# Kernel optimization log

Measured on AMD Instinct MI355X. Metric: run time of the kernel, lower is better.

Reference implementation:

```python
import jax, jax.numpy as jnp
import numpy as np

BLOCK_SIZE = 256
N_EMBD = 768
HEAD_SIZE = 768  # == n_embd so RoPE table (dim=n_embd) matches channel pairing


def _rope_tables(T, dim, theta0=10000.0):
    # compute_freq(dim=n_embd, seq_len=block_size, theta_0=10000):
    # theta_j = theta0^(-2j/dim), angle[t, j] = t * theta_j
    j = jnp.arange(dim // 2, dtype=jnp.float32)
    theta = jnp.float32(theta0) ** (-2.0 * j / jnp.float32(dim))
    ang = jnp.arange(T, dtype=jnp.float32)[:, None] * theta[None, :]  # [T, dim/2]
    return jnp.cos(ang), jnp.sin(ang)


def _apply_rope(t, cos, sin):
    # t: [B, T, D]; pair adjacent channels (2j, 2j+1) as complex, rotate.
    B, T, D = t.shape
    tr = t.reshape(B, T, D // 2, 2)
    re, im = tr[..., 0], tr[..., 1]
    out_re = re * cos[None] - im * sin[None]
    out_im = re * sin[None] + im * cos[None]
    return jnp.stack([out_re, out_im], axis=-1).reshape(B, T, D)


def setup_inputs() -> dict:
    key = jax.random.key(0)
    k1, k2, k3, k4 = jax.random.split(key, 4)
    B, T = 128, BLOCK_SIZE
    x = jax.random.normal(k1, (B, T, N_EMBD), dtype=jnp.float32)
    Wq = jax.random.normal(k2, (N_EMBD, HEAD_SIZE), dtype=jnp.float32) * 0.02
    Wk = jax.random.normal(k3, (N_EMBD, HEAD_SIZE), dtype=jnp.float32) * 0.02
    Wv = jax.random.normal(k4, (N_EMBD, HEAD_SIZE), dtype=jnp.float32) * 0.02
    return {"x": x, "Wq": Wq, "Wk": Wk, "Wv": Wv}


def reference(x, Wq, Wk, Wv):
    B, T, C = x.shape
    q = x @ Wq  # [B, T, D]
    k = x @ Wk
    v = x @ Wv
    cos, sin = _rope_tables(T, HEAD_SIZE)
    q = _apply_rope(q, cos, sin)
    k = _apply_rope(k, cos, sin)
    scale = jnp.float32(HEAD_SIZE) ** -0.5
    wei = jnp.einsum('bqd,bkd->bqk', q, k) * scale  # [B, T, T]
    causal = jnp.tril(jnp.ones((T, T), dtype=bool))
    wei = jnp.where(causal[None], wei, -jnp.inf)
    wei = jax.nn.softmax(wei, axis=-1)
    # dropout(p=0.2) is identity in eval/deterministic baseline
    out = jnp.einsum('bqk,bkd->bqd', wei, v)  # [B, T, D]
    return out
```

## Files before the change

kernel.cpp:

```cpp
#include <hip/hip_runtime.h>
#include <hip/hip_bf16.h>
#include <stdint.h>


typedef __attribute__((ext_vector_type(8))) short short8;
typedef __attribute__((ext_vector_type(4))) short short4v;
typedef __attribute__((ext_vector_type(4))) float f32x4;

__device__ __forceinline__ short f2bf(float f) {
    uint32_t u = __float_as_uint(f);
    u += 0x7fffu + ((u >> 16) & 1u);
    return (short)(u >> 16);
}

__global__ __launch_bounds__(256) void cvt_x(const float* __restrict__ x,
                                             short* __restrict__ xb) {
    long i = ((long)blockIdx.x * 256 + threadIdx.x) * 4;
    f32x4 v = *(const f32x4*)(x + i);
    short4v o;
    o.x = f2bf(v.x); o.y = f2bf(v.y); o.z = f2bf(v.z); o.w = f2bf(v.w);
    *(short4v*)(xb + i) = o;
}

__global__ __launch_bounds__(256) void cvt_wt(const float* __restrict__ W,
                                              short* __restrict__ Wt) {
    __shared__ float tile[32][33];
    int d0 = blockIdx.x * 32, c0 = blockIdx.y * 32;
    int tr = threadIdx.x >> 5, tc = threadIdx.x & 31;
    #pragma unroll
    for (int i = 0; i < 32; i += 8)
        tile[tr + i][tc] = W[(long)(c0 + tr + i) * 768 + d0 + tc];
    __syncthreads();
    #pragma unroll
    for (int i = 0; i < 32; i += 8)
        Wt[(long)(d0 + tr + i) * 768 + c0 + tc] = f2bf(tile[tc][tr + i]);
}

__global__ __launch_bounds__(256) void rope_tab(float2* __restrict__ rt) {
    int i = blockIdx.x * 256 + threadIdx.x;
    int t = i / 384, j = i - t * 384;
    const float CE = -0.034603417655f;
    float th = exp2f((float)j * CE);
    float s, c;
    sincosf((float)t * th, &s, &c);
    rt[i] = make_float2(c, s);
}

__global__ __launch_bounds__(512, 2)
void qkv256(const short* __restrict__ A, const short* __restrict__ B,
            short* __restrict__ Q, short* __restrict__ Kb,
            short* __restrict__ Vt, const float2* __restrict__ rt) {
    int p = blockIdx.x;
    int c = p & 7, j = p >> 3;
    int st = j / 9;
    int bx = j - st * 9;
    int by = c * 16 + st;
    const int m0 = by * 256, n0 = bx * 256;

    __shared__ short lA[2][256 * 64];
    __shared__ short lB[2][256 * 64];

    const int tid = threadIdx.x;
    const int w = tid >> 6, lane = tid & 63;
    const int wm = (w >> 2) * 128;
    const int wn = (w & 3) * 64;
    const int lr8 = lane >> 3;
    const int scol = (((lane & 7) - lr8) & 7) * 8;
    const int fr = lane & 15, kq = lane >> 4;

    f32x4 acc[8][4] = {};
    short8 af[4][2];
    short8 bq[4][2];

#define STAGE_HALF(lX, gX, r0g, h, t) do {                                     \
    int _buf = (t) & 1;                                                        \
    _Pragma("unroll")                                                          \
    for (int _i = 0; _i < 2; ++_i) {                                           \
        int _rl = (h) * 128 + (w * 2 + _i) * 8;                                \
        const short* _g = (gX) + (long)((r0g) + _rl + lr8) * 768               \
                               + (t) * 64 + scol;                              \
        __builtin_amdgcn_global_load_lds(                                      \
            (const __attribute__((address_space(1))) void*)_g,                 \
            (__attribute__((address_space(3))) void*)(&lX[_buf][_rl * 64]),    \
            16, 0, 0);                                                         \
    }                                                                          \
} while (0)

#define LOAD_A(mh, buf) do {                                                   \
    _Pragma("unroll")                                                          \
    for (int _t = 0; _t < 4; ++_t)                                             \
        _Pragma("unroll")                                                      \
        for (int _k = 0; _k < 2; ++_k)                                         \
            af[_t][_k] = *(const short8*)(&lA[buf][                            \
                (wm + (mh) * 64 + _t * 16 + fr) * 64 +                         \
                ((_k * 4 + kq + fr) & 7) * 8]);                                \
} while (0)

#define LOAD_B(nh, buf) do {                                                   \
    _Pragma("unroll")                                                          \
    for (int _t = 0; _t < 2; ++_t)                                             \
        _Pragma("unroll")                                                      \
        for (int _k = 0; _k < 2; ++_k)                                         \
            bq[(nh) * 2 + _t][_k] = *(const short8*)(&lB[buf][                 \
                (wn + (nh) * 32 + _t * 16 + fr) * 64 +                         \
                ((_k * 4 + kq + fr) & 7) * 8]);                                \
} while (0)

#define MMA_Q(mh, nh) do {                                                     \
    __builtin_amdgcn_s_setprio(1);                                             \
    _Pragma("unroll")                                                          \
    for (int _t = 0; _t < 4; ++_t)                                             \
        _Pragma("unroll")                                                      \
        for (int _n = 0; _n < 2; ++_n)                                         \
            _Pragma("unroll")                                                  \
            for (int _k = 0; _k < 2; ++_k)                                     \
                acc[(mh) * 4 + _t][(nh) * 2 + _n] =                            \
                    __builtin_amdgcn_mfma_f32_16x16x32_bf16(                   \
                        af[_t][_k], bq[(nh) * 2 + _n][_k],                     \
                        acc[(mh) * 4 + _t][(nh) * 2 + _n], 0, 0, 0);           \
    __builtin_amdgcn_s_setprio(0);                                             \
} while (0)

#define BAR() __builtin_amdgcn_s_barrier()
#define LGKM0() asm volatile("s_waitcnt lgkmcnt(0)" ::: "memory")
#define VMC4() asm volatile("s_waitcnt vmcnt(4)" ::: "memory")
#define VMC0() asm volatile("s_waitcnt vmcnt(0)" ::: "memory")

    STAGE_HALF(lB, B, n0, 0, 0);
    STAGE_HALF(lB, B, n0, 1, 0);
    STAGE_HALF(lA, A, m0, 0, 0);
    STAGE_HALF(lA, A, m0, 1, 0);
    STAGE_HALF(lB, B, n0, 0, 1);
    STAGE_HALF(lB, B, n0, 1, 1);
    VMC4();
    BAR();

    #pragma unroll 1
    for (int i = 0; i < 6; ++i) {
        const int t0 = 2 * i;
        const bool more = (i < 5);
        LOAD_A(0, 0); LOAD_B(0, 0);
        STAGE_HALF(lA, A, m0, 0, t0 + 1);
        BAR(); LGKM0(); MMA_Q(0, 0); BAR();
        LOAD_B(1, 0);
        STAGE_HALF(lA, A, m0, 1, t0 + 1);
        BAR(); LGKM0(); MMA_Q(0, 1); BAR();
        LOAD_A(1, 0);
        if (more) STAGE_HALF(lB, B, n0, 0, t0 + 2);
        BAR(); LGKM0(); MMA_Q(1, 1); BAR();
        if (more) STAGE_HALF(lB, B, n0, 1, t0 + 2);
        BAR(); LGKM0(); MMA_Q(1, 0);
        if (more) { VMC4(); } else { VMC0(); }
        BAR();
        LOAD_A(0, 1); LOAD_B(0, 1);
        if (more) STAGE_HALF(lA, A, m0, 0, t0 + 2);
        BAR(); LGKM0(); MMA_Q(0, 0); BAR();
        LOAD_B(1, 1);
        if (more) STAGE_HALF(lA, A, m0, 1, t0 + 2);
        BAR(); LGKM0(); MMA_Q(0, 1); BAR();
        LOAD_A(1, 1);
        if (more) STAGE_HALF(lB, B, n0, 0, t0 + 3);
        BAR(); LGKM0(); MMA_Q(1, 1); BAR();
        if (more) STAGE_HALF(lB, B, n0, 1, t0 + 3);
        BAR(); LGKM0(); MMA_Q(1, 0);
        if (more) VMC4();
        BAR();
    }

    const int type = (bx >= 6) ? 2 : (bx >= 3 ? 1 : 0);
    const int nl0 = n0 - type * 768;
    const int r0 = wm + (lane >> 4) * 4;
    const int c0 = wn + (lane & 15);
    if (type < 2) {
        short* dst = (type == 0) ? Q : Kb;
        const int par = lane & 1;
        #pragma unroll
        for (int tmi = 0; tmi < 8; ++tmi)
            #pragma unroll
            for (int tni = 0; tni < 4; ++tni) {
                int col = nl0 + c0 + tni * 16;
                const float2* rtc = rt + (col >> 1);
                #pragma unroll
                for (int r = 0; r < 4; ++r) {
                    int row = m0 + r0 + tmi * 16 + r;
                    float val = acc[tmi][tni][r];
                    float pv = __shfl_xor(val, 1);
                    float2 cs = rtc[(row & 255) * 384];
                    float re = par ? pv : val;
                    float im = par ? val : pv;
                    float o = par ? (re * cs.y + im * cs.x)
                                  : (re * cs.x - im * cs.y);
                    dst[(long)row * 768 + col] = f2bf(o);
                }
            }
    } else {
        #pragma unroll
        for (int tmi = 0; tmi < 8; ++tmi)
            #pragma unroll
            for (int tni = 0; tni < 4; ++tni) {
                int col = nl0 + c0 + tni * 16;
                #pragma unroll
                for (int r = 0; r < 4; ++r) {
                    int row = m0 + r0 + tmi * 16 + r;
                    Vt[((long)(row >> 8) * 768 + col) * 256 + (row & 255)] =
                        f2bf(acc[tmi][tni][r]);
                }
            }
    }
#undef STAGE_HALF
#undef LOAD_A
#undef LOAD_B
#undef MMA_Q
#undef BAR
#undef LGKM0
#undef VMC4
#undef VMC0
}

__global__ __launch_bounds__(512)
void attn_fused(const short* __restrict__ Qm, const short* __restrict__ Km,
                const short* __restrict__ Vm, float* __restrict__ out,
                float scale) {
    int p = blockIdx.x;
    int c = p & 7, j = p >> 3;
    int bz = c * 16 + (j >> 1);
    int mh = j & 1;
    const short* Ab = Qm + (long)bz * 196608 + (long)mh * 98304;
    const short* Bb = Km + (long)bz * 196608;
    const short* Vb = Vm + (long)bz * 196608;

    __shared__ short smem[67584];

    const int tid = threadIdx.x;
    const int w = tid >> 6, lane = tid & 63;
    const int wm = (w >> 2) * 64;
    const int wn = (w & 3) * 64;
    const int lr8 = lane >> 3;
    const int scol = (((lane & 7) - lr8) & 7) * 8;
    const int fr = lane & 15, kq = lane >> 4;
    const int cb = fr;

    f32x4 acc[4][4] = {};

#define GLL(g, l) __builtin_amdgcn_global_load_lds(                            \
        (const __attribute__((address_space(1))) void*)(g),                    \
        (__attribute__((address_space(3))) void*)(l), 16, 0, 0)

#define STAGE_QK(t) do { int _b = (t) & 1;                                     \
    _Pragma("unroll")                                                          \
    for (int _i = 0; _i < 2; ++_i) { int _s = _i * 8 + w;                      \
        GLL(Ab + (long)(_s * 8 + lr8) * 768 + (t) * 64 + scol,                 \
            smem + _b * 8192 + _s * 512); }                                    \
    _Pragma("unroll")                                                          \
    for (int _i = 0; _i < 4; ++_i) { int _s = _i * 8 + w;                      \
        GLL(Bb + (long)(_s * 8 + lr8) * 768 + (t) * 64 + scol,                 \
            smem + 16384 + _b * 16384 + _s * 512); } } while (0)

#define STAGE_V(dc, kc, b) do {                                                \
    _Pragma("unroll")                                                          \
    for (int _i = 0; _i < 2; ++_i) { int _s = _i * 8 + w;                      \
        GLL(Vb + (long)((dc) * 128 + _s * 8 + lr8) * 256 + (kc) * 64 + scol,   \
            smem + 49152 + (b) * 8192 + _s * 512); } } while (0)

    STAGE_QK(0);
    __syncthreads();
    #pragma unroll 1
    for (int t = 0; t < 12; ++t) {
        if (t < 11) STAGE_QK(t + 1);
        const short* la = smem + (t & 1) * 8192;
        const short* lb = smem + 16384 + (t & 1) * 16384;
        #pragma unroll
        for (int cc = 0; cc < 2; ++cc) {
            const int sphys = ((cc * 4 + kq + fr) & 7) * 8;
            short8 afr[4], bfr[4];
            #pragma unroll
            for (int tmi = 0; tmi < 4; ++tmi)
                afr[tmi] = *(const short8*)(la + (wm + fr + tmi * 16) * 64 + sphys);
            #pragma unroll
            for (int tni = 0; tni < 4; ++tni)
                bfr[tni] = *(const short8*)(lb + (wn + fr + tni * 16) * 64 + sphys);
            #pragma unroll
            for (int tmi = 0; tmi < 4; ++tmi)
                #pragma unroll
                for (int tni = 0; tni < 4; ++tni)
                    acc[tmi][tni] = __builtin_amdgcn_mfma_f32_16x16x32_bf16(
                        afr[tmi], bfr[tni], acc[tmi][tni], 0, 0, 0);
        }
        __syncthreads();
    }

    STAGE_V(0, 0, 0);

    const int r0 = kq * 4;
    const int nw = w & 3;
    float* redm = (float*)(smem + 65536);
    float* reds = redm + 512;

    float M[16];
    #pragma unroll
    for (int tmi = 0; tmi < 4; ++tmi)
        #pragma unroll
        for (int r = 0; r < 4; ++r) {
            int rowL = wm + tmi * 16 + r0 + r;
            int tloc = mh * 128 + rowL;
            float m = -1e30f;
            #pragma unroll
            for (int tni = 0; tni < 4; ++tni) {
                int col = wn + cb + tni * 16;
                float v = (col <= tloc) ? acc[tmi][tni][r] * scale : -1e30f;
                acc[tmi][tni][r] = v;
                m = fmaxf(m, v);
            }
            m = fmaxf(m, __shfl_xor(m, 1));
            m = fmaxf(m, __shfl_xor(m, 2));
            m = fmaxf(m, __shfl_xor(m, 4));
            m = fmaxf(m, __shfl_xor(m, 8));
            M[tmi * 4 + r] = m;
        }
    if (cb == 0) {
        #pragma unroll
        for (int tmi = 0; tmi < 4; ++tmi)
            #pragma unroll
            for (int r = 0; r < 4; ++r)
                redm[(wm + tmi * 16 + r0 + r) * 4 + nw] = M[tmi * 4 + r];
    }
    __syncthreads();
    #pragma unroll
    for (int tmi = 0; tmi < 4; ++tmi)
        #pragma unroll
        for (int r = 0; r < 4; ++r) {
            f32x4 v = *(const f32x4*)(redm + (wm + tmi * 16 + r0 + r) * 4);
            M[tmi * 4 + r] = fmaxf(fmaxf(v.x, v.y), fmaxf(v.z, v.w));
        }
    float Sm[16];
    #pragma unroll
    for (int tmi = 0; tmi < 4; ++tmi)
        #pragma unroll
        for (int r = 0; r < 4; ++r) {
            float mm = M[tmi * 4 + r];
            float s = 0.f;
            #pragma unroll
            for (int tni = 0; tni < 4; ++tni) {
                float e = __expf(acc[tmi][tni][r] - mm);
                acc[tmi][tni][r] = e;
                s += e;
            }
            s += __shfl_xor(s, 1);
            s += __shfl_xor(s, 2);
            s += __shfl_xor(s, 4);
            s += __shfl_xor(s, 8);
            Sm[tmi * 4 + r] = s;
        }
    if (cb == 0) {
        #pragma unroll
        for (int tmi = 0; tmi < 4; ++tmi)
            #pragma unroll
            for (int r = 0; r < 4; ++r)
                reds[(wm + tmi * 16 + r0 + r) * 4 + nw] = Sm[tmi * 4 + r];
    }
    __syncthreads();

    short* Pch = smem + (w & 3) * 8192;
    #pragma unroll
    for (int tmi = 0; tmi < 4; ++tmi)
        #pragma unroll
        for (int r = 0; r < 4; ++r) {
            int rowL = wm + tmi * 16 + r0 + r;
            f32x4 sv = *(const f32x4*)(reds + rowL * 4);
            float inv = 1.0f / (sv.x + sv.y + sv.z + sv.w);
            #pragma unroll
            for (int tni = 0; tni < 4; ++tni) {
                int l = (cb >> 3) + tni * 2;
                Pch[rowL * 64 + ((l + rowL) & 7) * 8 + (cb & 7)] =
                    f2bf(acc[tmi][tni][r] * inv);
            }
        }
    __syncthreads();

    const int kcN = mh ? 4 : 2;
    const int wn2 = (w & 3) * 32;
    const long rowB = (long)bz * 256 + (long)mh * 128;
    int vb = 0;
    #pragma unroll 1
    for (int dc = 0; dc < 6; ++dc) {
        f32x4 a2[4][2] = {};
        #pragma unroll 1
        for (int kc = 0; kc < kcN; ++kc) {
            int ndc = dc, nkc = kc + 1;
            if (nkc == kcN) { ndc = dc + 1; nkc = 0; }
            if (ndc < 6) STAGE_V(ndc, nkc, vb ^ 1);
            const short* pch = smem + kc * 8192;
            const short* lv = smem + 49152 + vb * 8192;
            #pragma unroll
            for (int cc = 0; cc < 2; ++cc) {
                const int sp = ((cc * 4 + kq + fr) & 7) * 8;
                short8 ap[4], bv[2];
                #pragma unroll
                for (int tmi = 0; tmi < 4; ++tmi)
                    ap[tmi] = *(const short8*)(pch + (wm + tmi * 16 + fr) * 64 + sp);
                #pragma unroll
                for (int tn = 0; tn < 2; ++tn)
                    bv[tn] = *(const short8*)(lv + (wn2 + tn * 16 + fr) * 64 + sp);
                #pragma unroll
                for (int tmi = 0; tmi < 4; ++tmi)
                    #pragma unroll
                    for (int tn = 0; tn < 2; ++tn)
                        a2[tmi][tn] = __builtin_amdgcn_mfma_f32_16x16x32_bf16(
                            ap[tmi], bv[tn], a2[tmi][tn], 0, 0, 0);
            }
            __syncthreads();
            vb ^= 1;
        }
        #pragma unroll
        for (int tmi = 0; tmi < 4; ++tmi)
            #pragma unroll
            for (int tn = 0; tn < 2; ++tn)
                #pragma unroll
                for (int r = 0; r < 4; ++r) {
                    long row = rowB + wm + tmi * 16 + kq * 4 + r;
                    int col = dc * 128 + wn2 + tn * 16 + cb;
                    out[row * 768 + col] = a2[tmi][tn][r];
                }
    }
#undef GLL
#undef STAGE_QK
#undef STAGE_V
}

extern "C" void kernel_launch(void* const* d_in, const int* in_sizes, int n_in,
                              void* d_out, int out_size, void* d_ws, size_t ws_size,
                              hipStream_t stream) {
    const float* x  = (const float*)d_in[0];
    const float* Wq = (const float*)d_in[1];
    const float* Wk = (const float*)d_in[2];
    const float* Wv = (const float*)d_in[3];

    char* ws = (char*)d_ws;
    short*  xb = (short*)(ws);
    short*  wt = (short*)(ws + 50331648);
    short*  qb = (short*)(ws + 53870592);
    short*  kb = (short*)(ws + 104202240);
    short*  vt = (short*)(ws + 154533888);
    float2* rt = (float2*)(ws + 255197184);

    cvt_x<<<24576, 256, 0, stream>>>(x, xb);
    dim3 gw(24, 24);
    cvt_wt<<<gw, 256, 0, stream>>>(Wq, wt);
    cvt_wt<<<gw, 256, 0, stream>>>(Wk, wt + 589824);
    cvt_wt<<<gw, 256, 0, stream>>>(Wv, wt + 1179648);
    rope_tab<<<384, 256, 0, stream>>>(rt);

    qkv256<<<1152, 512, 0, stream>>>(xb, wt, qb, kb, vt, rt);

    attn_fused<<<256, 512, 0, stream>>>(qb, kb, vt, (float*)d_out,
                                        0.0360843918f);
}
```

Before: 389.7 us.

## Split attention into 64-row query tiles skipping fully masked causal key chunks

Replaces the 128-query-row, 512-thread attention kernel with a 256-thread kernel handling 64 query rows per block, doubling the grid to 512 blocks. Each block only loads and multiplies the causally visible key chunks (qh+1 of 4), and waves beyond that chunk count sit idle during QK^T. Block order is mirrored across batch groups so the uneven per-block work spreads across CUs. This cuts wasted MFMA and load work on masked regions and lowers LDS use, at the cost of idle waves in short blocks and more blocks re-reading K/V.

```diff
diff --git a/kernel.cpp b/kernel.cpp
--- a/kernel.cpp
+++ b/kernel.cpp
@@ -217,28 +217,27 @@
 #undef VMC0
 }
 
-__global__ __launch_bounds__(512)
-void attn_fused(const short* __restrict__ Qm, const short* __restrict__ Km,
-                const short* __restrict__ Vm, float* __restrict__ out,
-                float scale) {
+__global__ __launch_bounds__(256)
+void attn2(const short* __restrict__ Qm, const short* __restrict__ Km,
+           const short* __restrict__ Vm, float* __restrict__ out,
+           float scale) {
     int p = blockIdx.x;
     int c = p & 7, j = p >> 3;
-    int bz = c * 16 + (j >> 1);
-    int mh = j & 1;
-    const short* Ab = Qm + (long)bz * 196608 + (long)mh * 98304;
+    int b = j >> 2, q0 = j & 3;
+    int qh = (b & 8) ? 3 - q0 : q0;
+    int bz = c * 16 + b;
+    const int NC = qh + 1;
+    const short* Ab = Qm + (long)bz * 196608 + (long)qh * 49152;
     const short* Bb = Km + (long)bz * 196608;
     const short* Vb = Vm + (long)bz * 196608;
 
-    __shared__ short smem[67584];
+    __shared__ short smem[40960];
 
     const int tid = threadIdx.x;
     const int w = tid >> 6, lane = tid & 63;
-    const int wm = (w >> 2) * 64;
-    const int wn = (w & 3) * 64;
     const int lr8 = lane >> 3;
     const int scol = (((lane & 7) - lr8) & 7) * 8;
     const int fr = lane & 15, kq = lane >> 4;
-    const int cb = fr;
 
     f32x4 acc[4][4] = {};
 
@@ -248,43 +247,44 @@
 
 #define STAGE_QK(t) do { int _b = (t) & 1;                                     \
     _Pragma("unroll")                                                          \
-    for (int _i = 0; _i < 2; ++_i) { int _s = _i * 8 + w;                      \
+    for (int _i = 0; _i < 2; ++_i) { int _s = _i * 4 + w;                      \
         GLL(Ab + (long)(_s * 8 + lr8) * 768 + (t) * 64 + scol,                 \
-            smem + _b * 8192 + _s * 512); }                                    \
-    _Pragma("unroll")                                                          \
-    for (int _i = 0; _i < 4; ++_i) { int _s = _i * 8 + w;                      \
+            smem + _b * 4096 + _s * 512); }                                    \
+    for (int _i = 0; _i < 2 * NC; ++_i) { int _s = _i * 4 + w;                 \
         GLL(Bb + (long)(_s * 8 + lr8) * 768 + (t) * 64 + scol,                 \
-            smem + 16384 + _b * 16384 + _s * 512); } } while (0)
-
-#define STAGE_V(dc, kc, b) do {                                                \
-    _Pragma("unroll")                                                          \
-    for (int _i = 0; _i < 2; ++_i) { int _s = _i * 8 + w;                      \
+            smem + 8192 + _b * 16384 + _s * 512); } } while (0)
+
+#define STAGE_V(dc, kc, vb) do {                                               \
+    _Pragma("unroll")                                                          \
+    for (int _i = 0; _i < 4; ++_i) { int _s = _i * 4 + w;                      \
         GLL(Vb + (long)((dc) * 128 + _s * 8 + lr8) * 256 + (kc) * 64 + scol,   \
-            smem + 49152 + (b) * 8192 + _s * 512); } } while (0)
+            smem + 16384 + (vb) * 8192 + _s * 512); } } while (0)
 
     STAGE_QK(0);
     __syncthreads();
     #pragma unroll 1
     for (int t = 0; t < 12; ++t) {
         if (t < 11) STAGE_QK(t + 1);
-        const short* la = smem + (t & 1) * 8192;
-        const short* lb = smem + 16384 + (t & 1) * 16384;
-        #pragma unroll
-        for (int cc = 0; cc < 2; ++cc) {
-            const int sphys = ((cc * 4 + kq + fr) & 7) * 8;
-            short8 afr[4], bfr[4];
-            #pragma unroll
-            for (int tmi = 0; tmi < 4; ++tmi)
-                afr[tmi] = *(const short8*)(la + (wm + fr + tmi * 16) * 64 + sphys);
-            #pragma unroll
-            for (int tni = 0; tni < 4; ++tni)
-                bfr[tni] = *(const short8*)(lb + (wn + fr + tni * 16) * 64 + sphys);
-            #pragma unroll
-            for (int tmi = 0; tmi < 4; ++tmi)
+        if (w < NC) {
+            const short* la = smem + (t & 1) * 4096;
+            const short* lb = smem + 8192 + (t & 1) * 16384 + w * 4096;
+            #pragma unroll
+            for (int cc = 0; cc < 2; ++cc) {
+                const int sp = ((cc * 4 + kq + fr) & 7) * 8;
+                short8 afr[4], bfr[4];
+                #pragma unroll
+                for (int tmi = 0; tmi < 4; ++tmi)
+                    afr[tmi] = *(const short8*)(la + (tmi * 16 + fr) * 64 + sp);
                 #pragma unroll
                 for (int tni = 0; tni < 4; ++tni)
-                    acc[tmi][tni] = __builtin_amdgcn_mfma_f32_16x16x32_bf16(
-                        afr[tmi], bfr[tni], acc[tmi][tni], 0, 0, 0);
+                    bfr[tni] = *(const short8*)(lb + (tni * 16 + fr) * 64 + sp);
+                #pragma unroll
+                for (int tmi = 0; tmi < 4; ++tmi)
+                    #pragma unroll
+                    for (int tni = 0; tni < 4; ++tni)
+                        acc[tmi][tni] = __builtin_amdgcn_mfma_f32_16x16x32_bf16(
+                            afr[tmi], bfr[tni], acc[tmi][tni], 0, 0, 0);
+            }
         }
         __syncthreads();
     }
@@ -292,21 +292,20 @@
     STAGE_V(0, 0, 0);
 
     const int r0 = kq * 4;
-    const int nw = w & 3;
-    float* redm = (float*)(smem + 65536);
-    float* reds = redm + 512;
+    float* redm = (float*)(smem + 32768);
+    float* reds = redm + 256;
 
     float M[16];
     #pragma unroll
     for (int tmi = 0; tmi < 4; ++tmi)
         #pragma unroll
         for (int r = 0; r < 4; ++r) {
-            int rowL = wm + tmi * 16 + r0 + r;
-            int tloc = mh * 128 + rowL;
+            int rowL = tmi * 16 + r0 + r;
+            int tloc = qh * 64 + rowL;
             float m = -1e30f;
             #pragma unroll
             for (int tni = 0; tni < 4; ++tni) {
-                int col = wn + cb + tni * 16;
+                int col = w * 64 + fr + tni * 16;
                 float v = (col <= tloc) ? acc[tmi][tni][r] * scale : -1e30f;
                 acc[tmi][tni][r] = v;
                 m = fmaxf(m, v);
@@ -317,19 +316,19 @@
             m = fmaxf(m, __shfl_xor(m, 8));
             M[tmi * 4 + r] = m;
         }
-    if (cb == 0) {
+    if (fr == 0) {
         #pragma unroll
         for (int tmi = 0; tmi < 4; ++tmi)
             #pragma unroll
             for (int r = 0; r < 4; ++r)
-                redm[(wm + tmi * 16 + r0 + r) * 4 + nw] = M[tmi * 4 + r];
+                redm[(tmi * 16 + r0 + r) * 4 + w] = M[tmi * 4 + r];
     }
     __syncthreads();
     #pragma unroll
     for (int tmi = 0; tmi < 4; ++tmi)
         #pragma unroll
         for (int r = 0; r < 4; ++r) {
-            f32x4 v = *(const f32x4*)(redm + (wm + tmi * 16 + r0 + r) * 4);
+            f32x4 v = *(const f32x4*)(redm + (tmi * 16 + r0 + r) * 4);
             M[tmi * 4 + r] = fmaxf(fmaxf(v.x, v.y), fmaxf(v.z, v.w));
         }
     float Sm[16];
@@ -351,53 +350,52 @@
             s += __shfl_xor(s, 8);
             Sm[tmi * 4 + r] = s;
         }
-    if (cb == 0) {
+    if (fr == 0) {
         #pragma unroll
         for (int tmi = 0; tmi < 4; ++tmi)
             #pragma unroll
             for (int r = 0; r < 4; ++r)
-                reds[(wm + tmi * 16 + r0 + r) * 4 + nw] = Sm[tmi * 4 + r];
+                reds[(tmi * 16 + r0 + r) * 4 + w] = Sm[tmi * 4 + r];
     }
     __syncthreads();
 
-    short* Pch = smem + (w & 3) * 8192;
+    short* Pch = smem + w * 4096;
     #pragma unroll
     for (int tmi = 0; tmi < 4; ++tmi)
         #pragma unroll
         for (int r = 0; r < 4; ++r) {
-            int rowL = wm + tmi * 16 + r0 + r;
+            int rowL = tmi * 16 + r0 + r;
             f32x4 sv = *(const f32x4*)(reds + rowL * 4);
             float inv = 1.0f / (sv.x + sv.y + sv.z + sv.w);
             #pragma unroll
             for (int tni = 0; tni < 4; ++tni) {
-                int l = (cb >> 3) + tni * 2;
-                Pch[rowL * 64 + ((l + rowL) & 7) * 8 + (cb & 7)] =
+                int l = (fr >> 3) + tni * 2;
+                Pch[rowL * 64 + ((l + rowL) & 7) * 8 + (fr & 7)] =
                     f2bf(acc[tmi][tni][r] * inv);
             }
         }
     __syncthreads();
 
-    const int kcN = mh ? 4 : 2;
-    const int wn2 = (w & 3) * 32;
-    const long rowB = (long)bz * 256 + (long)mh * 128;
+    const int wn2 = w * 32;
+    const long rowB = (long)bz * 256 + (long)qh * 64;
     int vb = 0;
     #pragma unroll 1
     for (int dc = 0; dc < 6; ++dc) {
         f32x4 a2[4][2] = {};
         #pragma unroll 1
-        for (int kc = 0; kc < kcN; ++kc) {
+        for (int kc = 0; kc < NC; ++kc) {
             int ndc = dc, nkc = kc + 1;
-            if (nkc == kcN) { ndc = dc + 1; nkc = 0; }
+            if (nkc == NC) { ndc = dc + 1; nkc = 0; }
             if (ndc < 6) STAGE_V(ndc, nkc, vb ^ 1);
-            const short* pch = smem + kc * 8192;
-            const short* lv = smem + 49152 + vb * 8192;
+            const short* pch = smem + kc * 4096;
+            const short* lv = smem + 16384 + vb * 8192;
             #pragma unroll
             for (int cc = 0; cc < 2; ++cc) {
                 const int sp = ((cc * 4 + kq + fr) & 7) * 8;
                 short8 ap[4], bv[2];
                 #pragma unroll
                 for (int tmi = 0; tmi < 4; ++tmi)
-                    ap[tmi] = *(const short8*)(pch + (wm + tmi * 16 + fr) * 64 + sp);
+                    ap[tmi] = *(const short8*)(pch + (tmi * 16 + fr) * 64 + sp);
                 #pragma unroll
                 for (int tn = 0; tn < 2; ++tn)
                     bv[tn] = *(const short8*)(lv + (wn2 + tn * 16 + fr) * 64 + sp);
@@ -417,8 +415,8 @@
             for (int tn = 0; tn < 2; ++tn)
                 #pragma unroll
                 for (int r = 0; r < 4; ++r) {
-                    long row = rowB + wm + tmi * 16 + kq * 4 + r;
-                    int col = dc * 128 + wn2 + tn * 16 + cb;
+                    long row = rowB + tmi * 16 + kq * 4 + r;
+                    int col = dc * 128 + wn2 + tn * 16 + fr;
                     out[row * 768 + col] = a2[tmi][tn][r];
                 }
     }
@@ -452,6 +450,5 @@
 
     qkv256<<<1152, 512, 0, stream>>>(xb, wt, qb, kb, vt, rt);
 
-    attn_fused<<<256, 512, 0, stream>>>(qb, kb, vt, (float*)d_out,
-                                        0.0360843918f);
-}
+    attn2<<<512, 256, 0, stream>>>(qb, kb, vt, (float*)d_out, 0.0360843918f);
+}
```

New measurement: 388.3 us. Within noise of the previous version (-0.3%).

## Merge prep kernels into one launch and deepen QKV GEMM prefetch

Applied to the files above, without the earlier changes.

Combines the x conversion, three weight-transpose conversions and the RoPE table kernel into a single prep launch that dispatches on block index, removing four kernel launches. In the QKV GEMM, global-to-LDS staging for both A and B halves of the next k-tile is issued earlier and grouped, and the wait count rises to vmcnt(8), so more loads are in flight during MFMA work. The change to the prefetch schedule keeps more outstanding loads per wave and moves when LDS buffers are overwritten, so its correctness relies on the barrier placement remaining valid.

```diff
diff --git a/kernel.cpp b/kernel.cpp
--- a/kernel.cpp
+++ b/kernel.cpp
@@ -13,37 +13,44 @@
     return (short)(u >> 16);
 }
 
-__global__ __launch_bounds__(256) void cvt_x(const float* __restrict__ x,
-                                             short* __restrict__ xb) {
-    long i = ((long)blockIdx.x * 256 + threadIdx.x) * 4;
-    f32x4 v = *(const f32x4*)(x + i);
-    short4v o;
-    o.x = f2bf(v.x); o.y = f2bf(v.y); o.z = f2bf(v.z); o.w = f2bf(v.w);
-    *(short4v*)(xb + i) = o;
-}
-
-__global__ __launch_bounds__(256) void cvt_wt(const float* __restrict__ W,
-                                              short* __restrict__ Wt) {
+__global__ __launch_bounds__(256)
+void prep(const float* __restrict__ x, const float* __restrict__ Wq,
+          const float* __restrict__ Wk, const float* __restrict__ Wv,
+          short* __restrict__ xb, short* __restrict__ wt,
+          float2* __restrict__ rt) {
     __shared__ float tile[32][33];
-    int d0 = blockIdx.x * 32, c0 = blockIdx.y * 32;
-    int tr = threadIdx.x >> 5, tc = threadIdx.x & 31;
-    #pragma unroll
-    for (int i = 0; i < 32; i += 8)
-        tile[tr + i][tc] = W[(long)(c0 + tr + i) * 768 + d0 + tc];
-    __syncthreads();
-    #pragma unroll
-    for (int i = 0; i < 32; i += 8)
-        Wt[(long)(d0 + tr + i) * 768 + c0 + tc] = f2bf(tile[tc][tr + i]);
-}
-
-__global__ __launch_bounds__(256) void rope_tab(float2* __restrict__ rt) {
-    int i = blockIdx.x * 256 + threadIdx.x;
-    int t = i / 384, j = i - t * 384;
-    const float CE = -0.034603417655f;
-    float th = exp2f((float)j * CE);
-    float s, c;
-    sincosf((float)t * th, &s, &c);
-    rt[i] = make_float2(c, s);
+    const int bid = blockIdx.x;
+    const int tid = threadIdx.x;
+    if (bid < 24576) {
+        long i = ((long)bid * 256 + tid) * 4;
+        f32x4 v = *(const f32x4*)(x + i);
+        short4v o;
+        o.x = f2bf(v.x); o.y = f2bf(v.y); o.z = f2bf(v.z); o.w = f2bf(v.w);
+        *(short4v*)(xb + i) = o;
+    } else if (bid < 26304) {
+        int r = bid - 24576;
+        int wsel = r / 576;
+        int t2 = r - wsel * 576;
+        const float* W = (wsel == 0) ? Wq : (wsel == 1 ? Wk : Wv);
+        short* Wt = wt + wsel * 589824;
+        int d0 = (t2 % 24) * 32, c0 = (t2 / 24) * 32;
+        int tr = tid >> 5, tc = tid & 31;
+        #pragma unroll
+        for (int i = 0; i < 32; i += 8)
+            tile[tr + i][tc] = W[(long)(c0 + tr + i) * 768 + d0 + tc];
+        __syncthreads();
+        #pragma unroll
+        for (int i = 0; i < 32; i += 8)
+            Wt[(long)(d0 + tr + i) * 768 + c0 + tc] = f2bf(tile[tc][tr + i]);
+    } else {
+        int i = (bid - 26304) * 256 + tid;
+        int t = i / 384, j = i - t * 384;
+        const float CE = -0.034603417655f;
+        float th = exp2f((float)j * CE);
+        float s, c;
+        sincosf((float)t * th, &s, &c);
+        rt[i] = make_float2(c, s);
+    }
 }
 
 __global__ __launch_bounds__(512, 2)
@@ -123,7 +130,7 @@
 
 #define BAR() __builtin_amdgcn_s_barrier()
 #define LGKM0() asm volatile("s_waitcnt lgkmcnt(0)" ::: "memory")
-#define VMC4() asm volatile("s_waitcnt vmcnt(4)" ::: "memory")
+#define VMC8() asm volatile("s_waitcnt vmcnt(8)" ::: "memory")
 #define VMC0() asm volatile("s_waitcnt vmcnt(0)" ::: "memory")
 
     STAGE_HALF(lB, B, n0, 0, 0);
@@ -132,7 +139,9 @@
     STAGE_HALF(lA, A, m0, 1, 0);
     STAGE_HALF(lB, B, n0, 0, 1);
     STAGE_HALF(lB, B, n0, 1, 1);
-    VMC4();
+    STAGE_HALF(lA, A, m0, 0, 1);
+    STAGE_HALF(lA, A, m0, 1, 1);
+    VMC8();
     BAR();
 
     #pragma unroll 1
@@ -140,30 +149,30 @@
         const int t0 = 2 * i;
         const bool more = (i < 5);
         LOAD_A(0, 0); LOAD_B(0, 0);
-        STAGE_HALF(lA, A, m0, 0, t0 + 1);
         BAR(); LGKM0(); MMA_Q(0, 0); BAR();
         LOAD_B(1, 0);
-        STAGE_HALF(lA, A, m0, 1, t0 + 1);
         BAR(); LGKM0(); MMA_Q(0, 1); BAR();
         LOAD_A(1, 0);
-        if (more) STAGE_HALF(lB, B, n0, 0, t0 + 2);
+        if (more) { STAGE_HALF(lB, B, n0, 0, t0 + 2);
+                    STAGE_HALF(lB, B, n0, 1, t0 + 2); }
         BAR(); LGKM0(); MMA_Q(1, 1); BAR();
-        if (more) STAGE_HALF(lB, B, n0, 1, t0 + 2);
+        if (more) { STAGE_HALF(lA, A, m0, 0, t0 + 2);
+                    STAGE_HALF(lA, A, m0, 1, t0 + 2); }
         BAR(); LGKM0(); MMA_Q(1, 0);
-        if (more) { VMC4(); } else { VMC0(); }
+        if (more) { VMC8(); } else { VMC0(); }
         BAR();
         LOAD_A(0, 1); LOAD_B(0, 1);
-        if (more) STAGE_HALF(lA, A, m0, 0, t0 + 2);
         BAR(); LGKM0(); MMA_Q(0, 0); BAR();
         LOAD_B(1, 1);
-        if (more) STAGE_HALF(lA, A, m0, 1, t0 + 2);
         BAR(); LGKM0(); MMA_Q(0, 1); BAR();
         LOAD_A(1, 1);
-        if (more) STAGE_HALF(lB, B, n0, 0, t0 + 3);
+        if (more) { STAGE_HALF(lB, B, n0, 0, t0 + 3);
+                    STAGE_HALF(lB, B, n0, 1, t0 + 3); }
         BAR(); LGKM0(); MMA_Q(1, 1); BAR();
-        if (more) STAGE_HALF(lB, B, n0, 1, t0 + 3);
+        if (more) { STAGE_HALF(lA, A, m0, 0, t0 + 3);
+                    STAGE_HALF(lA, A, m0, 1, t0 + 3); }
         BAR(); LGKM0(); MMA_Q(1, 0);
-        if (more) VMC4();
+        if (more) VMC8();
         BAR();
     }
 
@@ -213,7 +222,7 @@
 #undef MMA_Q
 #undef BAR
 #undef LGKM0
-#undef VMC4
+#undef VMC8
 #undef VMC0
 }
 
@@ -443,12 +452,7 @@
     short*  vt = (short*)(ws + 154533888);
     float2* rt = (float2*)(ws + 255197184);
 
-    cvt_x<<<24576, 256, 0, stream>>>(x, xb);
-    dim3 gw(24, 24);
-    cvt_wt<<<gw, 256, 0, stream>>>(Wq, wt);
-    cvt_wt<<<gw, 256, 0, stream>>>(Wk, wt + 589824);
-    cvt_wt<<<gw, 256, 0, stream>>>(Wv, wt + 1179648);
-    rope_tab<<<384, 256, 0, stream>>>(rt);
+    prep<<<26688, 256, 0, stream>>>(x, Wq, Wk, Wv, xb, wt, rt);
 
     qkv256<<<1152, 512, 0, stream>>>(xb, wt, qb, kb, vt, rt);
 
```

Result: no change. 385.4 us (-1.1%).
